# Optimization experiments

Hardware: AMD Instinct MI355X
Metric: run time of the kernel (lower is better)

## Reference

```python
import jax, jax.numpy as jnp
import numpy as np

B, D_IN, M, D_MEM = 65536, 64, 2048, 64


def setup_inputs() -> dict:
    key = jax.random.key(0)
    k = jax.random.split(key, 5)
    glorot = lambda kk, shape: jax.random.uniform(
        kk, shape, jnp.float32,
        -jnp.sqrt(6.0 / (shape[0] + shape[1])), jnp.sqrt(6.0 / (shape[0] + shape[1])))
    return {
        "inputs": jax.random.normal(k[0], (B, D_IN), jnp.float32),
        "W_att": glorot(k[1], (D_IN, M)),
        "b_att": jnp.zeros((M,), jnp.float32),
        "W_write": glorot(k[2], (D_IN, D_MEM)),
        "b_write": jnp.zeros((D_MEM,), jnp.float32),
        "memory": glorot(k[3], (M, D_MEM)),
        "update_gate": jnp.full((M,), 0.5, jnp.float32),
    }


def reference(inputs, W_att, b_att, W_write, b_write, memory, update_gate):
    # Read attention: Dense(memory_size, softmax) -> [B, M]
    read_attention = jax.nn.softmax(inputs @ W_att + b_att, axis=-1)
    # Read: [B, M] @ [M, Dm] -> [B, Dm]
    read_vector = read_attention @ memory
    # Write candidate: Dense(memory_dim, tanh) -> [B, Dm]
    candidate_write = jnp.tanh(inputs @ W_write + b_write)
    aggregated_write = jnp.mean(candidate_write, axis=0)[None, :]  # [1, Dm]
    write_attention = jnp.mean(read_attention, axis=0)             # [M]
    update_weights = (write_attention * update_gate)[:, None]      # [M, 1]
    # Gated in-place memory update (returned as new state)
    new_memory = memory * (1.0 - update_weights) + update_weights * aggregated_write
    return read_vector, new_memory
```

## Files before the change

kernel.cpp:

```cpp
#include <hip/hip_runtime.h>
#include <hip/hip_bf16.h>

typedef unsigned int   u32;
typedef unsigned short u16;

typedef __bf16 bf16x8 __attribute__((ext_vector_type(8)));
typedef float  f32x4  __attribute__((ext_vector_type(4)));
typedef u32    u32x4  __attribute__((ext_vector_type(4)));
typedef u32    u32x2  __attribute__((ext_vector_type(2)));

union Frag { u32x4 u; bf16x8 b; };

#define MFMA16 __builtin_amdgcn_mfma_f32_16x16x32_bf16

#define B_ROWS 65536
#define D_IN   64
#define M_SZ   2048
#define D_MEM  64

#define WT_OFF      0
#define MEMT_OFF    262144
#define WWT_OFF     524288
#define CSF_OFF     532480
#define AGF_OFF     540672
#define CSP_OFF     540928
#define AGP_OFF     8929536
#define WS_REQUIRED 9191680

#define L2E 1.4426950408889634f

#define AS1 __attribute__((address_space(1)))
#define AS3 __attribute__((address_space(3)))

#if defined(__has_builtin)
#if __has_builtin(__builtin_amdgcn_global_load_lds)
#define HAS_GLD 1
#endif
#endif
#ifndef HAS_GLD
#define HAS_GLD 0
#endif

__device__ __forceinline__ float bf2f(u16 h) { return __uint_as_float(((u32)h) << 16); }
__device__ __forceinline__ u16 f2bf(float f) {
    u32 u = __float_as_uint(f);
    return (u16)((u + 0x7FFFu + ((u >> 16) & 1u)) >> 16);
}
#if defined(__has_builtin) && __has_builtin(__builtin_amdgcn_exp2f)
__device__ __forceinline__ float exp2fast(float x) { return __builtin_amdgcn_exp2f(x); }
#else
__device__ __forceinline__ float exp2fast(float x) { return __expf(x * 0.6931471805599453f); }
#endif
__device__ __forceinline__ float tanh_fast(float x) {
    const float e = exp2fast(x * (2.0f * L2E));
    return 1.0f - 2.0f * __builtin_amdgcn_rcpf(e + 1.0f);
}
__device__ __forceinline__ bool detect_bf16(const void* ug) {
    return ((const u32*)ug)[0] == 0x3F003F00u;
}
__device__ __forceinline__ float load_elem(const void* p, size_t i, bool isbf) {
    return isbf ? bf2f(((const u16*)p)[i]) : ((const float*)p)[i];
}

__device__ __forceinline__ u32 cvtpk_bf16(float lo, float hi) {
    u32 r;
    asm("v_cvt_pk_bf16_f32 %0, %1, %2" : "=v"(r) : "v"(lo), "v"(hi));
    return r;
}
#if defined(__has_builtin) && __has_builtin(__builtin_amdgcn_permlane32_swap) && \
    __has_builtin(__builtin_amdgcn_permlane16_swap)
__device__ __forceinline__ void pl32swap(u32& a, u32& b) {
    u32x2 r = __builtin_amdgcn_permlane32_swap(a, b, false, false);
    a = r[0]; b = r[1];
}
__device__ __forceinline__ void pl16swap(u32& a, u32& b) {
    u32x2 r = __builtin_amdgcn_permlane16_swap(a, b, false, false);
    a = r[0]; b = r[1];
}
#else
__device__ __forceinline__ void pl32swap(u32& a, u32& b) {
    asm("v_permlane32_swap_b32 %0, %1" : "+v"(a), "+v"(b));
}
__device__ __forceinline__ void pl16swap(u32& a, u32& b) {
    asm("v_permlane16_swap_b32 %0, %1" : "+v"(a), "+v"(b));
}
#endif
template<int CTRL>
__device__ __forceinline__ float xadd(float v) {
    int x = __builtin_amdgcn_update_dpp(0, __float_as_int(v), CTRL, 0xF, 0xF, true);
    return v + __int_as_float(x);
}

__global__ void __launch_bounds__(256)
prep_kernel(const void* Watt, const void* mem_in, const void* Wwr, const void* ug,
            u16* Wt, u16* memT, u16* Wwt, float* CSF)
{
    const bool isbf = detect_bf16(ug);
    const int b = blockIdx.x;
    const int t = threadIdx.x;
    if (b == 65) {
        for (int i = t; i < 2112; i += 256) CSF[i] = 0.f;
        return;
    }
    __shared__ u16 tile[64][65];
    const void* src; u16* dst; int C, rb, cb, bsel;
    if (b < 32)      { src = Watt;   dst = Wt;   C = 2048; rb = 0;           cb = b * 64; bsel = 0; }
    else if (b < 64) { src = mem_in; dst = memT; C = 64;   rb = (b-32) * 64; cb = 0;      bsel = 1; }
    else             { src = Wwr;    dst = Wwt;  C = 64;   rb = 0;           cb = 0;      bsel = 2; }

#pragma unroll
    for (int j = 0; j < 16; ++j) {
        int e = j * 256 + t;
        int r = e >> 6, c = e & 63;
        float v = load_elem(src, (size_t)(rb + r) * C + cb + c, isbf);
        tile[r][c] = f2bf(v);
    }
    __syncthreads();
#pragma unroll
    for (int j = 0; j < 16; ++j) {
        int e = j * 256 + t;
        int c2 = e >> 6, r2 = e & 63;
        size_t di;
        if (bsel == 0) {
            const int m = cb + c2;
            const int k2 = (r2 & 7) | ((((r2 >> 3) ^ m) & 7) << 3);
            di = (size_t)m * 64 + k2;
        } else if (bsel == 1) {
            const int m2 = (r2 & 7) | ((((r2 >> 3) ^ c2) & 7) << 3);
            di = (size_t)c2 * 2048 + rb + m2;
        } else {
            di = (size_t)c2 * 64 + r2;
        }
        dst[di] = tile[r2][c2];
    }
}

__global__ void __launch_bounds__(256, 2)
main_kernel(const void* x_in, const void* batt_in, const void* bwrite_in,
            const u16* __restrict__ Wt, const u16* __restrict__ memT,
            const u16* __restrict__ Wwt, const void* ug,
            float* CSF, float* AGF, u16* cs_part, u16* ag_part,
            int use_part, void* out)
{
    const bool isbf = detect_bf16(ug);
    const int tid = threadIdx.x;
    const int lane = tid & 63, wave = tid >> 6;
    const int quad = lane >> 4, l4 = lane & 15;
    const int rowbase = blockIdx.x * 128;
    const int wrow = blockIdx.x * 4 + wave;

    __shared__ __align__(16) u16 WtL[2][128][64];
    __shared__ __align__(16) u16 MeL[2][64][128];
    __shared__ __align__(16) float battL[2048];

    const int wvu = __builtin_amdgcn_readfirstlane(wave);

    {
        const int i0 = tid * 8;
#pragma unroll
        for (int j = 0; j < 8; ++j)
            battL[i0 + j] = load_elem(batt_in, i0 + j, isbf) * L2E;
    }

    auto cp16 = [&](const char* gsrc_lane, char* lds_base_uniform) {
#if HAS_GLD
        __builtin_amdgcn_global_load_lds((const AS1 void*)gsrc_lane,
                                         (AS3 void*)lds_base_uniform, 16, 0, 0);
#else
        *(u32x4*)(lds_base_uniform + lane * 16) = *(const u32x4*)gsrc_lane;
#endif
    };
    const char* WtB = (const char*)Wt;
    const char* MeB = (const char*)memT;
    auto stageWt = [&](int ch, int b) {
        char* lb = (char*)&WtL[b][0][0] + wvu * 4096;
        const char* gb = WtB + (size_t)ch * 16384 + wvu * 4096 + lane * 16;
#pragma unroll
        for (int j = 0; j < 4; ++j)
            cp16(gb + j * 1024, lb + j * 1024);
    };
    auto stageMe = [&](int ch, int b) {
        char* lb = (char*)&MeL[b][0][0] + wvu * 4096;
        const char* gb = MeB + (size_t)(wvu * 16 + (lane >> 4)) * 4096
                             + ch * 256 + (lane & 15) * 16;
#pragma unroll
        for (int j = 0; j < 4; ++j)
            cp16(gb + (size_t)j * 16384, lb + j * 1024);
    };

    Frag a[2][2];
#pragma unroll
    for (int rg = 0; rg < 2; ++rg) {
        const int arow = rowbase + wave * 32 + rg * 16 + l4;
        if (isbf) {
            const u16* xp = (const u16*)x_in + (size_t)arow * 64 + quad * 8;
            a[rg][0].u = *(const u32x4*)xp;
            a[rg][1].u = *(const u32x4*)(xp + 32);
        } else {
            const float* xp = (const float*)x_in + (size_t)arow * 64 + quad * 8;
#pragma unroll
            for (int j = 0; j < 8; ++j) {
                ((u16*)&a[rg][0])[j] = f2bf(xp[j]);
                ((u16*)&a[rg][1])[j] = f2bf(xp[32 + j]);
            }
        }
    }
    const f32x4 zf = {0.f, 0.f, 0.f, 0.f};

    stageWt(0, 0);

    float agout = 0.f;
    {
        f32x4 accW[4][2];
#pragma unroll
        for (int t = 0; t < 4; ++t) {
            const u16* bp = Wwt + (size_t)(t * 16 + l4) * 64 + quad * 8;
            Frag b0, b1; b0.u = *(const u32x4*)bp; b1.u = *(const u32x4*)(bp + 32);
#pragma unroll
            for (int rg = 0; rg < 2; ++rg) {
                accW[t][rg] = MFMA16(a[rg][0].b, b0.b, zf, 0, 0, 0);
                accW[t][rg] = MFMA16(a[rg][1].b, b1.b, accW[t][rg], 0, 0, 0);
            }
        }
#pragma unroll
        for (int t = 0; t < 4; ++t) {
            const float bw = load_elem(bwrite_in, t * 16 + l4, isbf);
            float s = 0.f;
#pragma unroll
            for (int rg = 0; rg < 2; ++rg)
#pragma unroll
                for (int i = 0; i < 4; ++i) s += tanh_fast(accW[t][rg][i] + bw);
            s += __shfl_xor(s, 16, 64);
            s += __shfl_xor(s, 32, 64);
            if (quad == t) agout = s;
        }
    }
    if (use_part) ag_part[wrow * 64 + lane] = f2bf(agout);
    else          atomicAdd(&AGF[lane], agout);

    __syncthreads();

    float lsum[2] = {0.f, 0.f};
    for (int ch = 0; ch < 16; ++ch) {
        const int cur = ch & 1;
        if (ch < 15) stageWt(ch + 1, cur ^ 1);
        for (int half = 0; half < 2; ++half) {
            const int mb = half * 64;
            const int mbase = ch * 128 + mb;
            Frag wb0[4], wb1[4]; f32x4 blv[4];
#pragma unroll
            for (int t = 0; t < 4; ++t) {
                const int rr = mb + t * 16 + l4, swr = rr & 7;
                wb0[t].u = *(const u32x4*)&WtL[cur][rr][(quad ^ swr) << 3];
                wb1[t].u = *(const u32x4*)&WtL[cur][rr][((quad + 4) ^ swr) << 3];
                blv[t] = *(const f32x4*)&battL[mbase + t * 16 + quad * 4];
            }
#pragma unroll
            for (int t = 0; t < 4; ++t)
#pragma unroll
                for (int rg = 0; rg < 2; ++rg) {
                    f32x4 acc = MFMA16(wb0[t].b, a[rg][0].b, zf, 0, 0, 0);
                    acc = MFMA16(wb1[t].b, a[rg][1].b, acc, 0, 0, 0);
#pragma unroll
                    for (int i = 0; i < 4; ++i)
                        lsum[rg] += exp2fast(fmaf(acc[i], L2E, blv[t][i]));
                }
        }
        __syncthreads();
    }
    float invl[2];
#pragma unroll
    for (int rg = 0; rg < 2; ++rg) {
        float v = lsum[rg];
        v += __shfl_xor(v, 16, 64);
        v += __shfl_xor(v, 32, 64);
        invl[rg] = 1.f / v;
    }

    f32x4 oaccT[2][4] = {{zf,zf,zf,zf},{zf,zf,zf,zf}};
    stageMe(15, 1);
    __syncthreads();
    const bool sb0 = (l4 & 1), sb1 = (l4 & 2), sb2 = (l4 & 4), sb3 = (l4 & 8);
    for (int ch = 15; ch >= 0; --ch) {
        const int cur = ch & 1;
        if (ch > 0) { stageWt(ch - 1, cur ^ 1); stageMe(ch - 1, cur ^ 1); }
        for (int half = 0; half < 2; ++half) {
            const int mb = half * 64;
            const int mbase = ch * 128 + mb;
            const int mbh8 = mb >> 3;
            Frag wb0[4], wb1[4], mb0[4], mb1[4]; f32x4 blv[4];
#pragma unroll
            for (int t = 0; t < 4; ++t) {
                const int rr = mb + t * 16 + l4, swr = rr & 7;
                wb0[t].u = *(const u32x4*)&WtL[cur][rr][(quad ^ swr) << 3];
                wb1[t].u = *(const u32x4*)&WtL[cur][rr][((quad + 4) ^ swr) << 3];
                const int dd = t * 16 + l4, swd = dd & 7;
                mb0[t].u = *(const u32x4*)&MeL[cur][dd][(mbh8 | (quad ^ swd)) << 3];
                mb1[t].u = *(const u32x4*)&MeL[cur][dd][(mbh8 | ((quad + 4) ^ swd)) << 3];
                blv[t] = *(const f32x4*)&battL[mbase + t * 16 + quad * 4];
            }
            u32 P0[2][4], P1[2][4];
            float c16[16];
#pragma unroll
            for (int j = 0; j < 16; ++j) c16[j] = 0.f;
#pragma unroll
            for (int t = 0; t < 4; ++t)
#pragma unroll
                for (int rg = 0; rg < 2; ++rg) {
                    f32x4 acc = MFMA16(wb0[t].b, a[rg][0].b, zf, 0, 0, 0);
                    acc = MFMA16(wb1[t].b, a[rg][1].b, acc, 0, 0, 0);
                    const float il = invl[rg];
                    const float e0 = exp2fast(fmaf(acc[0], L2E, blv[t][0]));
                    const float e1 = exp2fast(fmaf(acc[1], L2E, blv[t][1]));
                    const float e2 = exp2fast(fmaf(acc[2], L2E, blv[t][2]));
                    const float e3 = exp2fast(fmaf(acc[3], L2E, blv[t][3]));
                    c16[t * 4 + 0] = fmaf(e0, il, c16[t * 4 + 0]);
                    c16[t * 4 + 1] = fmaf(e1, il, c16[t * 4 + 1]);
                    c16[t * 4 + 2] = fmaf(e2, il, c16[t * 4 + 2]);
                    c16[t * 4 + 3] = fmaf(e3, il, c16[t * 4 + 3]);
                    P0[rg][t] = cvtpk_bf16(e0, e1);
                    P1[rg][t] = cvtpk_bf16(e2, e3);
                }
            __builtin_amdgcn_s_setprio(1);
#pragma unroll
            for (int rg = 0; rg < 2; ++rg)
#pragma unroll
                for (int cc2 = 0; cc2 < 2; ++cc2) {
                    u32 b0 = P0[rg][2 * cc2], b2 = P0[rg][2 * cc2 + 1];
                    u32 b1 = P1[rg][2 * cc2], b3 = P1[rg][2 * cc2 + 1];
                    pl32swap(b0, b2); pl16swap(b0, b2);
                    pl32swap(b1, b3); pl16swap(b1, b3);
                    Frag bf; bf.u = (u32x4){b0, b1, b2, b3};
#pragma unroll
                    for (int dt = 0; dt < 4; ++dt) {
                        if (cc2 == 0)
                            oaccT[rg][dt] = MFMA16(mb0[dt].b, bf.b, oaccT[rg][dt], 0, 0, 0);
                        else
                            oaccT[rg][dt] = MFMA16(mb1[dt].b, bf.b, oaccT[rg][dt], 0, 0, 0);
                    }
                }
            __builtin_amdgcn_s_setprio(0);
            float u8[8];
#pragma unroll
            for (int k = 0; k < 8; ++k) {
                const float t0 = xadd<0xB1>(c16[2 * k]);
                const float t1 = xadd<0xB1>(c16[2 * k + 1]);
                u8[k] = sb0 ? t1 : t0;
            }
            float v4[4];
#pragma unroll
            for (int k = 0; k < 4; ++k) {
                const float t0 = xadd<0x4E>(u8[2 * k]);
                const float t1 = xadd<0x4E>(u8[2 * k + 1]);
                v4[k] = sb1 ? t1 : t0;
            }
            float w2[2];
#pragma unroll
            for (int k = 0; k < 2; ++k) {
                const float t0 = xadd<0x128>(v4[2 * k]);
                const float t1 = xadd<0x128>(v4[2 * k + 1]);
                w2[k] = sb3 ? t1 : t0;
            }
            const float f0 = w2[0] + __shfl_xor(w2[0], 4, 64);
            const float f1 = w2[1] + __shfl_xor(w2[1], 4, 64);
            const float csv = sb2 ? f1 : f0;
            const int tsel = ((l4 >> 3) & 1) | (((l4 >> 2) & 1) << 1);
            const int mout = mbase + tsel * 16 + quad * 4 + (l4 & 3);
            if (use_part) cs_part[(size_t)wrow * 2048 + mout] = f2bf(csv);
            else          atomicAdd(&CSF[mout], csv);
        }
        __syncthreads();
    }

#pragma unroll
    for (int rg = 0; rg < 2; ++rg)
#pragma unroll
        for (int dt = 0; dt < 4; ++dt) {
            const int gr = rowbase + wave * 32 + rg * 16 + l4;
            const int d0 = dt * 16 + quad * 4;
            const f32x4 o = oaccT[rg][dt] * invl[rg];
            if (isbf) {
                u32x2 w;
                w.x = cvtpk_bf16(o[0], o[1]);
                w.y = cvtpk_bf16(o[2], o[3]);
                *(u32x2*)&((u16*)out)[(size_t)gr * 64 + d0] = w;
            } else {
                *(f32x4*)&((float*)out)[(size_t)gr * 64 + d0] = o;
            }
        }
}

__global__ void __launch_bounds__(256)
tail_kernel(const u16* __restrict__ cs_part, const u16* __restrict__ ag_part,
            const void* mem_in, const void* ug, void* out)
{
    const bool isbf = detect_bf16(ug);
    const int b = blockIdx.x, t = threadIdx.x;
    __shared__ float agL[4][64];
    __shared__ float csL[32][8];
    {
        const int d = t & 63, seg = t >> 6;
        float s = 0.f;
        for (int k = 0; k < 512; ++k)
            s += bf2f(ag_part[(size_t)(seg * 512 + k) * 64 + d]);
        agL[seg][d] = s;
    }
    {
        const int m_loc = t >> 3, seg8 = t & 7;
        const int m = b * 32 + m_loc;
        float s = 0.f;
        for (int k = 0; k < 256; ++k)
            s += bf2f(cs_part[(size_t)(seg8 * 256 + k) * 2048 + m]);
        csL[m_loc][seg8] = s;
    }
    __syncthreads();
    const int m_loc = t >> 3, m = b * 32 + m_loc, d0 = (t & 7) * 8;
    float cs = 0.f;
#pragma unroll
    for (int k = 0; k < 8; ++k) cs += csL[m_loc][k];
    const float wa = cs * (1.f / 65536.f);
    const float uw = wa * load_elem(ug, m, isbf);
#pragma unroll
    for (int j = 0; j < 8; ++j) {
        const int d = d0 + j;
        const float ag = agL[0][d] + agL[1][d] + agL[2][d] + agL[3][d];
        const float agg = ag * (1.f / 65536.f);
        const size_t idx = (size_t)m * 64 + d;
        const float mv = load_elem(mem_in, idx, isbf);
        const float nm = mv * (1.f - uw) + uw * agg;
        if (isbf) ((u16*)out)[(size_t)4194304 + idx] = f2bf(nm);
        else      ((float*)out)[(size_t)4194304 + idx] = nm;
    }
}

__global__ void __launch_bounds__(256)
finalize_kernel(const void* mem_in, const void* ug,
                const float* __restrict__ CSF, const float* __restrict__ AGF,
                void* out)
{
    const bool isbf = detect_bf16(ug);
    const int idx = blockIdx.x * 256 + threadIdx.x;
    const int m = idx >> 6, d = idx & 63;
    const float wa  = CSF[m] * (1.f / 65536.f);
    const float agg = AGF[d] * (1.f / 65536.f);
    const float uw  = wa * load_elem(ug, m, isbf);
    const float mv  = load_elem(mem_in, idx, isbf);
    const float nm  = mv * (1.f - uw) + uw * agg;
    if (isbf) ((u16*)out)[(size_t)4194304 + idx] = f2bf(nm);
    else      ((float*)out)[(size_t)4194304 + idx] = nm;
}

extern "C" void kernel_launch(void* const* d_in, const int* in_sizes, int n_in,
                              void* d_out, int out_size, void* d_ws, size_t ws_size,
                              hipStream_t stream)
{
    (void)in_sizes; (void)n_in; (void)out_size;
    const void* x    = d_in[0];
    const void* Watt = d_in[1];
    const void* batt = d_in[2];
    const void* Wwr  = d_in[3];
    const void* bwr  = d_in[4];
    const void* mem  = d_in[5];
    const void* ug   = d_in[6];

    char* ws = (char*)d_ws;
    u16*   Wt      = (u16*)(ws + WT_OFF);
    u16*   memT    = (u16*)(ws + MEMT_OFF);
    u16*   Wwt     = (u16*)(ws + WWT_OFF);
    float* CSF     = (float*)(ws + CSF_OFF);
    float* AGF     = (float*)(ws + AGF_OFF);
    u16*   cs_part = (u16*)(ws + CSP_OFF);
    u16*   ag_part = (u16*)(ws + AGP_OFF);
    const int use_part = (ws_size >= (size_t)WS_REQUIRED) ? 1 : 0;

    prep_kernel<<<66, 256, 0, stream>>>(Watt, mem, Wwr, ug, Wt, memT, Wwt, CSF);
    main_kernel<<<512, 256, 0, stream>>>(x, batt, bwr, Wt, memT, Wwt, ug,
                                         CSF, AGF, cs_part, ag_part,
                                         use_part, d_out);
    if (use_part)
        tail_kernel<<<64, 256, 0, stream>>>(cs_part, ag_part, mem, ug, d_out);
    else
        finalize_kernel<<<512, 256, 0, stream>>>(mem, ug, CSF, AGF, d_out);
}
```

Baseline: 196.3 us.

## Restructure main kernel to 8 waves of 16 rows with LDS-aggregated atomics

Each wave now handles 16 rows instead of 32, and blocks grow to 512 threads, so the grid keeps 128 rows per block while getting more waves per CU and fewer registers per thread. Column sums and the write aggregate are first accumulated in shared memory with LDS atomics, then flushed once per block to global atomics. This replaces the bf16 partial buffers and the tail reduction kernel. The pre-scaled attention bias is computed once in the prep kernel and read from global memory instead of being staged into LDS by every block. The cost is that each Wt/memory tile loaded into LDS is reused across fewer rows per wave, and there are many LDS and global float atomics whose summation order is nondeterministic.

```diff
diff --git a/kernel.cpp b/kernel.cpp
--- a/kernel.cpp
+++ b/kernel.cpp
@@ -23,9 +23,7 @@
 #define WWT_OFF     524288
 #define CSF_OFF     532480
 #define AGF_OFF     540672
-#define CSP_OFF     540928
-#define AGP_OFF     8929536
-#define WS_REQUIRED 9191680
+#define BATTS_OFF   540928
 
 #define L2E 1.4426950408889634f
 
@@ -92,14 +90,17 @@
 }
 
 __global__ void __launch_bounds__(256)
-prep_kernel(const void* Watt, const void* mem_in, const void* Wwr, const void* ug,
-            u16* Wt, u16* memT, u16* Wwt, float* CSF)
+prep_kernel(const void* Watt, const void* mem_in, const void* Wwr,
+            const void* batt_in, const void* ug,
+            u16* Wt, u16* memT, u16* Wwt, float* CSF, float* battS)
 {
     const bool isbf = detect_bf16(ug);
     const int b = blockIdx.x;
     const int t = threadIdx.x;
     if (b == 65) {
         for (int i = t; i < 2112; i += 256) CSF[i] = 0.f;
+        for (int i = t; i < 2048; i += 256)
+            battS[i] = load_elem(batt_in, i, isbf) * L2E;
         return;
     }
     __shared__ u16 tile[64][65];
@@ -135,32 +136,25 @@
     }
 }
 
-__global__ void __launch_bounds__(256, 2)
-main_kernel(const void* x_in, const void* batt_in, const void* bwrite_in,
+__global__ void __launch_bounds__(512, 4)
+main_kernel(const void* x_in, const void* bwrite_in,
             const u16* __restrict__ Wt, const u16* __restrict__ memT,
-            const u16* __restrict__ Wwt, const void* ug,
-            float* CSF, float* AGF, u16* cs_part, u16* ag_part,
-            int use_part, void* out)
+            const u16* __restrict__ Wwt, const float* __restrict__ battS,
+            const void* ug, float* CSF, float* AGF, void* out)
 {
     const bool isbf = detect_bf16(ug);
     const int tid = threadIdx.x;
     const int lane = tid & 63, wave = tid >> 6;
     const int quad = lane >> 4, l4 = lane & 15;
     const int rowbase = blockIdx.x * 128;
-    const int wrow = blockIdx.x * 4 + wave;
-
-    __shared__ __align__(16) u16 WtL[2][128][64];
+
+    __shared__ __align__(16) u16 WtA[2][8192];
     __shared__ __align__(16) u16 MeL[2][64][128];
-    __shared__ __align__(16) float battL[2048];
+    __shared__ float csA[2112];
 
     const int wvu = __builtin_amdgcn_readfirstlane(wave);
 
-    {
-        const int i0 = tid * 8;
-#pragma unroll
-        for (int j = 0; j < 8; ++j)
-            battL[i0 + j] = load_elem(batt_in, i0 + j, isbf) * L2E;
-    }
+    for (int i = tid; i < 2112; i += 512) csA[i] = 0.f;
 
     auto cp16 = [&](const char* gsrc_lane, char* lds_base_uniform) {
 #if HAS_GLD
@@ -170,38 +164,36 @@
         *(u32x4*)(lds_base_uniform + lane * 16) = *(const u32x4*)gsrc_lane;
 #endif
     };
-    const char* WtB = (const char*)Wt;
-    const char* MeB = (const char*)memT;
     auto stageWt = [&](int ch, int b) {
-        char* lb = (char*)&WtL[b][0][0] + wvu * 4096;
-        const char* gb = WtB + (size_t)ch * 16384 + wvu * 4096 + lane * 16;
-#pragma unroll
-        for (int j = 0; j < 4; ++j)
-            cp16(gb + j * 1024, lb + j * 1024);
+        char* lb = (char*)&WtA[b][0] + wvu * 2048;
+        const char* gb = (const char*)Wt + (size_t)ch * 16384 + wvu * 2048 + lane * 16;
+        cp16(gb, lb);
+        cp16(gb + 1024, lb + 1024);
     };
     auto stageMe = [&](int ch, int b) {
-        char* lb = (char*)&MeL[b][0][0] + wvu * 4096;
-        const char* gb = MeB + (size_t)(wvu * 16 + (lane >> 4)) * 4096
-                             + ch * 256 + (lane & 15) * 16;
-#pragma unroll
-        for (int j = 0; j < 4; ++j)
-            cp16(gb + (size_t)j * 16384, lb + j * 1024);
+#pragma unroll
+        for (int j = 0; j < 2; ++j) {
+            const int d = wvu * 8 + j * 4 + (lane >> 4);
+            const char* gb = (const char*)memT + (size_t)d * 4096
+                           + (size_t)ch * 256 + (lane & 15) * 16;
+            char* lb = (char*)&MeL[b][wvu * 8 + j * 4][0];
+            cp16(gb, lb);
+        }
     };
 
-    Frag a[2][2];
-#pragma unroll
-    for (int rg = 0; rg < 2; ++rg) {
-        const int arow = rowbase + wave * 32 + rg * 16 + l4;
+    Frag a[2];
+    {
+        const int arow = rowbase + wave * 16 + l4;
         if (isbf) {
             const u16* xp = (const u16*)x_in + (size_t)arow * 64 + quad * 8;
-            a[rg][0].u = *(const u32x4*)xp;
-            a[rg][1].u = *(const u32x4*)(xp + 32);
+            a[0].u = *(const u32x4*)xp;
+            a[1].u = *(const u32x4*)(xp + 32);
         } else {
             const float* xp = (const float*)x_in + (size_t)arow * 64 + quad * 8;
 #pragma unroll
             for (int j = 0; j < 8; ++j) {
-                ((u16*)&a[rg][0])[j] = f2bf(xp[j]);
-                ((u16*)&a[rg][1])[j] = f2bf(xp[32 + j]);
+                ((u16*)&a[0])[j] = f2bf(xp[j]);
+                ((u16*)&a[1])[j] = f2bf(xp[32 + j]);
             }
         }
     }
@@ -211,36 +203,30 @@
 
     float agout = 0.f;
     {
-        f32x4 accW[4][2];
+        f32x4 accW[4];
 #pragma unroll
         for (int t = 0; t < 4; ++t) {
             const u16* bp = Wwt + (size_t)(t * 16 + l4) * 64 + quad * 8;
             Frag b0, b1; b0.u = *(const u32x4*)bp; b1.u = *(const u32x4*)(bp + 32);
-#pragma unroll
-            for (int rg = 0; rg < 2; ++rg) {
-                accW[t][rg] = MFMA16(a[rg][0].b, b0.b, zf, 0, 0, 0);
-                accW[t][rg] = MFMA16(a[rg][1].b, b1.b, accW[t][rg], 0, 0, 0);
-            }
+            accW[t] = MFMA16(a[0].b, b0.b, zf, 0, 0, 0);
+            accW[t] = MFMA16(a[1].b, b1.b, accW[t], 0, 0, 0);
         }
 #pragma unroll
         for (int t = 0; t < 4; ++t) {
             const float bw = load_elem(bwrite_in, t * 16 + l4, isbf);
             float s = 0.f;
 #pragma unroll
-            for (int rg = 0; rg < 2; ++rg)
-#pragma unroll
-                for (int i = 0; i < 4; ++i) s += tanh_fast(accW[t][rg][i] + bw);
+            for (int i = 0; i < 4; ++i) s += tanh_fast(accW[t][i] + bw);
             s += __shfl_xor(s, 16, 64);
             s += __shfl_xor(s, 32, 64);
             if (quad == t) agout = s;
         }
     }
-    if (use_part) ag_part[wrow * 64 + lane] = f2bf(agout);
-    else          atomicAdd(&AGF[lane], agout);
 
     __syncthreads();
-
-    float lsum[2] = {0.f, 0.f};
+    atomicAdd(&csA[2048 + lane], agout);
+
+    float lsum = 0.f;
     for (int ch = 0; ch < 16; ++ch) {
         const int cur = ch & 1;
         if (ch < 15) stageWt(ch + 1, cur ^ 1);
@@ -251,33 +237,30 @@
 #pragma unroll
             for (int t = 0; t < 4; ++t) {
                 const int rr = mb + t * 16 + l4, swr = rr & 7;
-                wb0[t].u = *(const u32x4*)&WtL[cur][rr][(quad ^ swr) << 3];
-                wb1[t].u = *(const u32x4*)&WtL[cur][rr][((quad + 4) ^ swr) << 3];
-                blv[t] = *(const f32x4*)&battL[mbase + t * 16 + quad * 4];
-            }
-#pragma unroll
-            for (int t = 0; t < 4; ++t)
-#pragma unroll
-                for (int rg = 0; rg < 2; ++rg) {
-                    f32x4 acc = MFMA16(wb0[t].b, a[rg][0].b, zf, 0, 0, 0);
-                    acc = MFMA16(wb1[t].b, a[rg][1].b, acc, 0, 0, 0);
-#pragma unroll
-                    for (int i = 0; i < 4; ++i)
-                        lsum[rg] += exp2fast(fmaf(acc[i], L2E, blv[t][i]));
-                }
+                wb0[t].u = *(const u32x4*)&WtA[cur][rr * 64 + ((quad ^ swr) << 3)];
+                wb1[t].u = *(const u32x4*)&WtA[cur][rr * 64 + (((quad + 4) ^ swr) << 3)];
+                blv[t] = *(const f32x4*)&battS[mbase + t * 16 + quad * 4];
+            }
+#pragma unroll
+            for (int t = 0; t < 4; ++t) {
+                f32x4 acc = MFMA16(wb0[t].b, a[0].b, zf, 0, 0, 0);
+                acc = MFMA16(wb1[t].b, a[1].b, acc, 0, 0, 0);
+#pragma unroll
+                for (int i = 0; i < 4; ++i)
+                    lsum += exp2fast(fmaf(acc[i], L2E, blv[t][i]));
+            }
         }
         __syncthreads();
     }
-    float invl[2];
-#pragma unroll
-    for (int rg = 0; rg < 2; ++rg) {
-        float v = lsum[rg];
+    float invl;
+    {
+        float v = lsum;
         v += __shfl_xor(v, 16, 64);
         v += __shfl_xor(v, 32, 64);
-        invl[rg] = 1.f / v;
-    }
-
-    f32x4 oaccT[2][4] = {{zf,zf,zf,zf},{zf,zf,zf,zf}};
+        invl = 1.f / v;
+    }
+
+    f32x4 oaccT[4] = {zf, zf, zf, zf};
     stageMe(15, 1);
     __syncthreads();
     const bool sb0 = (l4 & 1), sb1 = (l4 & 2), sb2 = (l4 & 4), sb3 = (l4 & 8);
@@ -292,54 +275,47 @@
 #pragma unroll
             for (int t = 0; t < 4; ++t) {
                 const int rr = mb + t * 16 + l4, swr = rr & 7;
-                wb0[t].u = *(const u32x4*)&WtL[cur][rr][(quad ^ swr) << 3];
-                wb1[t].u = *(const u32x4*)&WtL[cur][rr][((quad + 4) ^ swr) << 3];
+                wb0[t].u = *(const u32x4*)&WtA[cur][rr * 64 + ((quad ^ swr) << 3)];
+                wb1[t].u = *(const u32x4*)&WtA[cur][rr * 64 + (((quad + 4) ^ swr) << 3)];
                 const int dd = t * 16 + l4, swd = dd & 7;
                 mb0[t].u = *(const u32x4*)&MeL[cur][dd][(mbh8 | (quad ^ swd)) << 3];
                 mb1[t].u = *(const u32x4*)&MeL[cur][dd][(mbh8 | ((quad + 4) ^ swd)) << 3];
-                blv[t] = *(const f32x4*)&battL[mbase + t * 16 + quad * 4];
-            }
-            u32 P0[2][4], P1[2][4];
+                blv[t] = *(const f32x4*)&battS[mbase + t * 16 + quad * 4];
+            }
+            u32 P0[4], P1[4];
             float c16[16];
 #pragma unroll
             for (int j = 0; j < 16; ++j) c16[j] = 0.f;
 #pragma unroll
-            for (int t = 0; t < 4; ++t)
-#pragma unroll
-                for (int rg = 0; rg < 2; ++rg) {
-                    f32x4 acc = MFMA16(wb0[t].b, a[rg][0].b, zf, 0, 0, 0);
-                    acc = MFMA16(wb1[t].b, a[rg][1].b, acc, 0, 0, 0);
-                    const float il = invl[rg];
-                    const float e0 = exp2fast(fmaf(acc[0], L2E, blv[t][0]));
-                    const float e1 = exp2fast(fmaf(acc[1], L2E, blv[t][1]));
-                    const float e2 = exp2fast(fmaf(acc[2], L2E, blv[t][2]));
-                    const float e3 = exp2fast(fmaf(acc[3], L2E, blv[t][3]));
-                    c16[t * 4 + 0] = fmaf(e0, il, c16[t * 4 + 0]);
-                    c16[t * 4 + 1] = fmaf(e1, il, c16[t * 4 + 1]);
-                    c16[t * 4 + 2] = fmaf(e2, il, c16[t * 4 + 2]);
-                    c16[t * 4 + 3] = fmaf(e3, il, c16[t * 4 + 3]);
-                    P0[rg][t] = cvtpk_bf16(e0, e1);
-                    P1[rg][t] = cvtpk_bf16(e2, e3);
+            for (int t = 0; t < 4; ++t) {
+                f32x4 acc = MFMA16(wb0[t].b, a[0].b, zf, 0, 0, 0);
+                acc = MFMA16(wb1[t].b, a[1].b, acc, 0, 0, 0);
+                const float e0 = exp2fast(fmaf(acc[0], L2E, blv[t][0]));
+                const float e1 = exp2fast(fmaf(acc[1], L2E, blv[t][1]));
+                const float e2 = exp2fast(fmaf(acc[2], L2E, blv[t][2]));
+                const float e3 = exp2fast(fmaf(acc[3], L2E, blv[t][3]));
+                c16[t * 4 + 0] = fmaf(e0, invl, c16[t * 4 + 0]);
+                c16[t * 4 + 1] = fmaf(e1, invl, c16[t * 4 + 1]);
+                c16[t * 4 + 2] = fmaf(e2, invl, c16[t * 4 + 2]);
+                c16[t * 4 + 3] = fmaf(e3, invl, c16[t * 4 + 3]);
+                P0[t] = cvtpk_bf16(e0, e1);
+                P1[t] = cvtpk_bf16(e2, e3);
+            }
+#pragma unroll
+            for (int cc2 = 0; cc2 < 2; ++cc2) {
+                u32 b0 = P0[2 * cc2], b2 = P0[2 * cc2 + 1];
+                u32 b1 = P1[2 * cc2], b3 = P1[2 * cc2 + 1];
+                pl32swap(b0, b2); pl16swap(b0, b2);
+                pl32swap(b1, b3); pl16swap(b1, b3);
+                Frag bf; bf.u = (u32x4){b0, b1, b2, b3};
+#pragma unroll
+                for (int dt = 0; dt < 4; ++dt) {
+                    if (cc2 == 0)
+                        oaccT[dt] = MFMA16(mb0[dt].b, bf.b, oaccT[dt], 0, 0, 0);
+                    else
+                        oaccT[dt] = MFMA16(mb1[dt].b, bf.b, oaccT[dt], 0, 0, 0);
                 }
-            __builtin_amdgcn_s_setprio(1);
-#pragma unroll
-            for (int rg = 0; rg < 2; ++rg)
-#pragma unroll
-                for (int cc2 = 0; cc2 < 2; ++cc2) {
-                    u32 b0 = P0[rg][2 * cc2], b2 = P0[rg][2 * cc2 + 1];
-                    u32 b1 = P1[rg][2 * cc2], b3 = P1[rg][2 * cc2 + 1];
-                    pl32swap(b0, b2); pl16swap(b0, b2);
-                    pl32swap(b1, b3); pl16swap(b1, b3);
-                    Frag bf; bf.u = (u32x4){b0, b1, b2, b3};
-#pragma unroll
-                    for (int dt = 0; dt < 4; ++dt) {
-                        if (cc2 == 0)
-                            oaccT[rg][dt] = MFMA16(mb0[dt].b, bf.b, oaccT[rg][dt], 0, 0, 0);
-                        else
-                            oaccT[rg][dt] = MFMA16(mb1[dt].b, bf.b, oaccT[rg][dt], 0, 0, 0);
-                    }
-                }
-            __builtin_amdgcn_s_setprio(0);
+            }
             float u8[8];
 #pragma unroll
             for (int k = 0; k < 8; ++k) {
@@ -366,70 +342,27 @@
             const float csv = sb2 ? f1 : f0;
             const int tsel = ((l4 >> 3) & 1) | (((l4 >> 2) & 1) << 1);
             const int mout = mbase + tsel * 16 + quad * 4 + (l4 & 3);
-            if (use_part) cs_part[(size_t)wrow * 2048 + mout] = f2bf(csv);
-            else          atomicAdd(&CSF[mout], csv);
+            atomicAdd(&csA[mout], csv);
         }
         __syncthreads();
     }
 
-#pragma unroll
-    for (int rg = 0; rg < 2; ++rg)
-#pragma unroll
-        for (int dt = 0; dt < 4; ++dt) {
-            const int gr = rowbase + wave * 32 + rg * 16 + l4;
-            const int d0 = dt * 16 + quad * 4;
-            const f32x4 o = oaccT[rg][dt] * invl[rg];
-            if (isbf) {
-                u32x2 w;
-                w.x = cvtpk_bf16(o[0], o[1]);
-                w.y = cvtpk_bf16(o[2], o[3]);
-                *(u32x2*)&((u16*)out)[(size_t)gr * 64 + d0] = w;
-            } else {
-                *(f32x4*)&((float*)out)[(size_t)gr * 64 + d0] = o;
-            }
-        }
-}
-
-__global__ void __launch_bounds__(256)
-tail_kernel(const u16* __restrict__ cs_part, const u16* __restrict__ ag_part,
-            const void* mem_in, const void* ug, void* out)
-{
-    const bool isbf = detect_bf16(ug);
-    const int b = blockIdx.x, t = threadIdx.x;
-    __shared__ float agL[4][64];
-    __shared__ float csL[32][8];
-    {
-        const int d = t & 63, seg = t >> 6;
-        float s = 0.f;
-        for (int k = 0; k < 512; ++k)
-            s += bf2f(ag_part[(size_t)(seg * 512 + k) * 64 + d]);
-        agL[seg][d] = s;
-    }
-    {
-        const int m_loc = t >> 3, seg8 = t & 7;
-        const int m = b * 32 + m_loc;
-        float s = 0.f;
-        for (int k = 0; k < 256; ++k)
-            s += bf2f(cs_part[(size_t)(seg8 * 256 + k) * 2048 + m]);
-        csL[m_loc][seg8] = s;
-    }
-    __syncthreads();
-    const int m_loc = t >> 3, m = b * 32 + m_loc, d0 = (t & 7) * 8;
-    float cs = 0.f;
-#pragma unroll
-    for (int k = 0; k < 8; ++k) cs += csL[m_loc][k];
-    const float wa = cs * (1.f / 65536.f);
-    const float uw = wa * load_elem(ug, m, isbf);
-#pragma unroll
-    for (int j = 0; j < 8; ++j) {
-        const int d = d0 + j;
-        const float ag = agL[0][d] + agL[1][d] + agL[2][d] + agL[3][d];
-        const float agg = ag * (1.f / 65536.f);
-        const size_t idx = (size_t)m * 64 + d;
-        const float mv = load_elem(mem_in, idx, isbf);
-        const float nm = mv * (1.f - uw) + uw * agg;
-        if (isbf) ((u16*)out)[(size_t)4194304 + idx] = f2bf(nm);
-        else      ((float*)out)[(size_t)4194304 + idx] = nm;
+    for (int i = tid; i < 2048; i += 512) atomicAdd(&CSF[i], csA[i]);
+    if (tid < 64) atomicAdd(&AGF[tid], csA[2048 + tid]);
+
+#pragma unroll
+    for (int dt = 0; dt < 4; ++dt) {
+        const int gr = rowbase + wave * 16 + l4;
+        const int d0 = dt * 16 + quad * 4;
+        const f32x4 o = oaccT[dt] * invl;
+        if (isbf) {
+            u32x2 w;
+            w.x = cvtpk_bf16(o[0], o[1]);
+            w.y = cvtpk_bf16(o[2], o[3]);
+            *(u32x2*)&((u16*)out)[(size_t)gr * 64 + d0] = w;
+        } else {
+            *(f32x4*)&((float*)out)[(size_t)gr * 64 + d0] = o;
+        }
     }
 }
 
@@ -454,7 +387,7 @@
                               void* d_out, int out_size, void* d_ws, size_t ws_size,
                               hipStream_t stream)
 {
-    (void)in_sizes; (void)n_in; (void)out_size;
+    (void)in_sizes; (void)n_in; (void)out_size; (void)ws_size;
     const void* x    = d_in[0];
     const void* Watt = d_in[1];
     const void* batt = d_in[2];
@@ -464,21 +397,16 @@
     const void* ug   = d_in[6];
 
     char* ws = (char*)d_ws;
-    u16*   Wt      = (u16*)(ws + WT_OFF);
-    u16*   memT    = (u16*)(ws + MEMT_OFF);
-    u16*   Wwt     = (u16*)(ws + WWT_OFF);
-    float* CSF     = (float*)(ws + CSF_OFF);
-    float* AGF     = (float*)(ws + AGF_OFF);
-    u16*   cs_part = (u16*)(ws + CSP_OFF);
-    u16*   ag_part = (u16*)(ws + AGP_OFF);
-    const int use_part = (ws_size >= (size_t)WS_REQUIRED) ? 1 : 0;
-
-    prep_kernel<<<66, 256, 0, stream>>>(Watt, mem, Wwr, ug, Wt, memT, Wwt, CSF);
-    main_kernel<<<512, 256, 0, stream>>>(x, batt, bwr, Wt, memT, Wwt, ug,
-                                         CSF, AGF, cs_part, ag_part,
-                                         use_part, d_out);
-    if (use_part)
-        tail_kernel<<<64, 256, 0, stream>>>(cs_part, ag_part, mem, ug, d_out);
-    else
-        finalize_kernel<<<512, 256, 0, stream>>>(mem, ug, CSF, AGF, d_out);
-}
+    u16*   Wt    = (u16*)(ws + WT_OFF);
+    u16*   memT  = (u16*)(ws + MEMT_OFF);
+    u16*   Wwt   = (u16*)(ws + WWT_OFF);
+    float* CSF   = (float*)(ws + CSF_OFF);
+    float* AGF   = (float*)(ws + AGF_OFF);
+    float* battS = (float*)(ws + BATTS_OFF);
+
+    prep_kernel<<<66, 256, 0, stream>>>(Watt, mem, Wwr, batt, ug,
+                                        Wt, memT, Wwt, CSF, battS);
+    main_kernel<<<512, 512, 0, stream>>>(x, bwr, Wt, memT, Wwt, battS, ug,
+                                         CSF, AGF, d_out);
+    finalize_kernel<<<512, 256, 0, stream>>>(mem, ug, CSF, AGF, d_out);
+}
```

After: 203.5 us. 1.04x slower.
